# Optimization experiments

Hardware: AMD Instinct MI355X
Metric: run time of the kernel (lower is better)

The kernel has to match this reference:

```python
import jax, jax.numpy as jnp
import numpy as np

B, C, H, W = 4, 512, 32, 32
NUM_HEADS, DIM_HEAD = 16, 32
DIM_ATTN = NUM_HEADS * DIM_HEAD  # 512
N = H * W


def setup_inputs() -> dict:
    key = jax.random.key(0)
    ks = jax.random.split(key, 6)
    s = 0.02
    return {
        "x": jax.random.normal(ks[0], (B, C, H, W), jnp.float32),
        "w_qkv": jax.random.normal(ks[1], (3 * DIM_ATTN, C), jnp.float32) * s,
        "b_qkv": jax.random.normal(ks[2], (3 * DIM_ATTN,), jnp.float32) * s,
        "w_proj": jax.random.normal(ks[3], (C, DIM_ATTN), jnp.float32) * s,
        "b_proj": jax.random.normal(ks[4], (C,), jnp.float32) * s,
        "shared_rel_pos": jax.random.normal(ks[5], (1, NUM_HEADS, N, N), jnp.float32) * s,
    }


def reference(x, w_qkv, b_qkv, w_proj, b_proj, shared_rel_pos):
    b, c, h, w = x.shape
    n = h * w
    scale = DIM_HEAD ** -0.5
    # 1x1 conv == per-pixel matmul over channels
    qkv = jnp.einsum('bchw,oc->bohw', x, w_qkv) + b_qkv[None, :, None, None]
    # [B, heads, 3*dh, N] -> chunk along dim 2 (matches torch .chunk(3, dim=2))
    qkv = qkv.reshape(b, NUM_HEADS, 3 * DIM_HEAD, n)
    q, k, v = jnp.split(qkv, 3, axis=2)          # each [B, heads, dh, N]
    attn = jnp.einsum('bhdi,bhdj->bhij', q, k) * scale  # q^T @ k
    attn = attn + shared_rel_pos
    attn = jax.nn.softmax(attn, axis=-1)
    out = jnp.einsum('bhdj,bhij->bhdi', v, attn)  # v @ attn^T, [B, heads, dh, N]
    out = out.reshape(b, NUM_HEADS * DIM_HEAD, h, w)
    out = jnp.einsum('bchw,oc->bohw', out, w_proj) + b_proj[None, :, None, None]
    return out
```

## Files before the change

### kernel.cpp

```cpp
#include <hip/hip_runtime.h>
#include <cstdint>
#include <cstddef>

#define BATCH 4
#define CIN   512
#define NPIX  1024
#define HEADS 16
#define DH    32
#define DATTN 512
#define O_QKV 1536
#define PPAD  88

typedef unsigned short u16;
typedef __bf16 bf16x4 __attribute__((ext_vector_type(4)));
typedef __bf16 bf16x8 __attribute__((ext_vector_type(8)));
typedef float  f32x4  __attribute__((ext_vector_type(4)));

typedef const __attribute__((address_space(1))) void g1_t;
typedef __attribute__((address_space(3))) void l3_t;

#if defined(__has_builtin)
#if __has_builtin(__builtin_amdgcn_exp2f)
#define EXP2(x) __builtin_amdgcn_exp2f(x)
#endif
#endif
#ifndef EXP2
#define EXP2(x) __expf((x) * 0.6931471805599453f)
#endif

__device__ __forceinline__ u16 f2bf(float f) {
  unsigned u = __float_as_uint(f);
  u += 0x7fffu + ((u >> 16) & 1u);
  return (u16)(u >> 16);
}

__device__ __forceinline__ void gl_lds16(const void* gp, void* lp) {
  __builtin_amdgcn_global_load_lds((g1_t*)gp, (l3_t*)lp, 16, 0, 0);
}

__global__ __launch_bounds__(256) void prep_w(const float* __restrict__ w1,
                                              const float* __restrict__ w2,
                                              u16* __restrict__ o1,
                                              u16* __restrict__ o2) {
  const int idx = blockIdx.x * 256 + threadIdx.x;
  const int n1 = (O_QKV * CIN) >> 2;
  float4 v = (idx < n1) ? reinterpret_cast<const float4*>(w1)[idx]
                        : reinterpret_cast<const float4*>(w2)[idx - n1];
  uint2 pk = make_uint2((unsigned)f2bf(v.x) | ((unsigned)f2bf(v.y) << 16),
                        (unsigned)f2bf(v.z) | ((unsigned)f2bf(v.w) << 16));
  if (idx < n1) reinterpret_cast<uint2*>(o1)[idx] = pk;
  else          reinterpret_cast<uint2*>(o2)[idx - n1] = pk;
}

__global__ __launch_bounds__(256) void prep_x(const float* __restrict__ x,
                                              u16* __restrict__ xt) {
  __shared__ float sT[64][65];
  const int t  = threadIdx.x;
  const int n0 = blockIdx.x * 64;
  const int c0 = blockIdx.y * 64;
  const int b  = blockIdx.z;
  const float* xb = x + ((size_t)b * CIN + c0) * NPIX + n0;
#pragma unroll
  for (int i = 0; i < 4; ++i) {
    int r   = i * 16 + (t >> 4);
    int col = (t & 15) << 2;
    float4 v = *reinterpret_cast<const float4*>(&xb[(size_t)r * NPIX + col]);
    sT[r][col + 0] = v.x; sT[r][col + 1] = v.y;
    sT[r][col + 2] = v.z; sT[r][col + 3] = v.w;
  }
  __syncthreads();
#pragma unroll
  for (int i = 0; i < 2; ++i) {
    int nl = t >> 2;
    int ch = (t & 3) + (i << 2);
    u16 tmp[8];
#pragma unroll
    for (int e = 0; e < 8; ++e) tmp[e] = f2bf(sT[(ch << 3) + e][nl]);
    *reinterpret_cast<uint4*>(&xt[((size_t)b * NPIX + n0 + nl) * CIN + c0 + (ch << 3)]) =
        *reinterpret_cast<uint4*>(tmp);
  }
}

__global__ __launch_bounds__(256) void gemm_qkv_mfma(const u16* __restrict__ wq,
                                                     const u16* __restrict__ xt,
                                                     const float* __restrict__ bias,
                                                     u16* __restrict__ qt,
                                                     u16* __restrict__ kt,
                                                     u16* __restrict__ vt) {
  __shared__ __align__(16) u16 sA[96 * 64];
  __shared__ __align__(16) u16 sB[128 * 64];
  const int t  = threadIdx.x;
  const int w  = t >> 6, l = t & 63, g = l >> 4, ln = l & 15;
  const int n0 = blockIdx.x * 128;
  const int h  = blockIdx.y;
  const int b  = blockIdx.z;
  const int wm = w >> 1, wn = w & 1;

  const u16* wbase = wq + (size_t)h * 96 * CIN;
  const u16* xbase = xt + ((size_t)b * NPIX + n0) * CIN;

  f32x4 acc[3][4];
#pragma unroll
  for (int mi = 0; mi < 3; ++mi)
#pragma unroll
    for (int ni = 0; ni < 4; ++ni) acc[mi][ni] = {0.f, 0.f, 0.f, 0.f};

  for (int k0 = 0; k0 < CIN; k0 += 64) {
#pragma unroll
    for (int i = 0; i < 3; ++i) {
      int chunk = i * 256 + (w << 6) + l;
      gl_lds16(wbase + ((size_t)(chunk >> 3)) * CIN + k0 + ((chunk & 7) << 3),
               (char*)sA + i * 4096 + (w << 10));
    }
#pragma unroll
    for (int i = 0; i < 4; ++i) {
      int chunk = i * 256 + (w << 6) + l;
      gl_lds16(xbase + ((size_t)(chunk >> 3)) * CIN + k0 + ((chunk & 7) << 3),
               (char*)sB + i * 4096 + (w << 10));
    }
    __syncthreads();
#pragma unroll
    for (int kk = 0; kk < 64; kk += 32) {
      bf16x8 af[3], bfr[4];
#pragma unroll
      for (int mi = 0; mi < 3; ++mi)
        af[mi] = *reinterpret_cast<const bf16x8*>(&sA[(48 * wm + 16 * mi + ln) * 64 + kk + (g << 3)]);
#pragma unroll
      for (int ni = 0; ni < 4; ++ni)
        bfr[ni] = *reinterpret_cast<const bf16x8*>(&sB[((wn << 6) + (ni << 4) + ln) * 64 + kk + (g << 3)]);
#pragma unroll
      for (int mi = 0; mi < 3; ++mi)
#pragma unroll
        for (int ni = 0; ni < 4; ++ni)
          acc[mi][ni] = __builtin_amdgcn_mfma_f32_16x16x32_bf16(af[mi], bfr[ni], acc[mi][ni], 0, 0, 0);
    }
    __syncthreads();
  }

  const float QSC = 0.17677669529663687f * 1.4426950408889634f;
  const float* bh = bias + h * 96;
#pragma unroll
  for (int mi = 0; mi < 3; ++mi) {
    const int sec = 48 * wm + 16 * mi;
    const int rb  = sec + (g << 2);
    const float b0 = bh[rb + 0], b1 = bh[rb + 1], b2 = bh[rb + 2], b3 = bh[rb + 3];
#pragma unroll
    for (int ni = 0; ni < 4; ++ni) {
      const int n = n0 + (wn << 6) + (ni << 4) + ln;
      f32x4 a = acc[mi][ni];
      float v0 = a[0] + b0, v1 = a[1] + b1, v2 = a[2] + b2, v3 = a[3] + b3;
      if (sec < 32) { v0 *= QSC; v1 *= QSC; v2 *= QSC; v3 *= QSC; }
      u16 e0 = f2bf(v0), e1 = f2bf(v1), e2 = f2bf(v2), e3 = f2bf(v3);
      if (sec < 32) {
        const int d = sec + (g << 2);
        uint2 pk = make_uint2((unsigned)e0 | ((unsigned)e1 << 16),
                              (unsigned)e2 | ((unsigned)e3 << 16));
        *reinterpret_cast<uint2*>(&qt[(((size_t)(b * HEADS + h)) * NPIX + n) * DH + d]) = pk;
      } else if (sec < 64) {
        const int d = sec - 32 + (g << 2);
        uint2 pk = make_uint2((unsigned)e0 | ((unsigned)e1 << 16),
                              (unsigned)e2 | ((unsigned)e3 << 16));
        *reinterpret_cast<uint2*>(&kt[(((size_t)(b * HEADS + h)) * NPIX + n) * DH + d]) = pk;
      } else {
        const int d = sec - 64 + (g << 2);
        u16* vp = &vt[(((size_t)(b * HEADS + h)) * DH + d) * NPIX + n];
        vp[0] = e0; vp[NPIX] = e1; vp[2 * NPIX] = e2; vp[3 * NPIX] = e3;
      }
    }
  }
}

__global__ __launch_bounds__(512, 4) void attn_mfma(const u16* __restrict__ qt,
                                                    const u16* __restrict__ kt,
                                                    const u16* __restrict__ vt,
                                                    const float* __restrict__ rel,
                                                    u16* __restrict__ aout) {
  __shared__ __align__(16) u16 sK[2][2 * 2048];
  __shared__ __align__(16) u16 sV[2][2 * 2048];
  __shared__ __align__(16) u16 sP[8][16 * PPAD];

  const int t  = threadIdx.x;
  const int w  = t >> 6, l = t & 63, g = l >> 4, ln = l & 15;
  const int bid = blockIdx.x;
  const int xcd = bid & 7, sl = bid >> 3;
  const int h   = (xcd << 1) | (sl >> 5);
  const int i0  = ((sl >> 1) & 15) << 6;
  const int bp  = sl & 1;
  const int bw  = (bp << 1) | (w >> 2);
  const int iw  = w & 3;
  const float LOG2E = 1.4426950408889634f;

  bf16x8 qf = *reinterpret_cast<const bf16x8*>(
      qt + (((size_t)(bw * HEADS + h)) * NPIX + i0 + (iw << 4) + ln) * DH + (g << 3));

  f32x4 vzero = {0.f, 0.f, 0.f, 0.f};
  f32x4 accO[2] = {vzero, vzero};
  float l_lane[4] = {0.f, 0.f, 0.f, 0.f};

  const int sc_b  = (bp << 1) | (t >> 8);
  const int sc_cb = t & 255;
  const int sc_r  = sc_cb >> 3;
  const int sc_kc = (sc_cb & 7) ^ (sc_r & 7) ^ ((sc_r >> 3) & 1);
  const int sc_vc = (sc_cb & 7) ^ (sc_r & 7);
  const u16* ksrc0 = kt + (((size_t)(sc_b * HEADS + h)) * NPIX +
                           ((sc_r << 1) | (sc_kc >> 2))) * DH + ((sc_kc & 3) << 3);
  const u16* vsrc0 = vt + (((size_t)(sc_b * HEADS + h)) * DH + sc_r) * NPIX + (sc_vc << 3);

#define STAGE(js_, p_) do {                                               \
    gl_lds16(ksrc0 + (size_t)(js_) * 2048, (char*)&sK[p_][0] + (w << 10)); \
    gl_lds16(vsrc0 + (size_t)(js_) * 64,   (char*)&sV[p_][0] + (w << 10)); \
  } while (0)

  const float* relp = rel + ((size_t)h * NPIX + i0 + (iw << 4) + (g << 2)) * NPIX + (ln << 2);
  f32x4 relA4[4], relB4[4];
#pragma unroll
  for (int v = 0; v < 4; ++v)
    relA4[v] = *reinterpret_cast<const f32x4*>(relp + (size_t)v * NPIX);

  STAGE(0, 0);

  u16* sPw = &sP[w][0];
  const int lb = w >> 2;

  for (int js = 0; js < 16; ++js) {
    const int p = js & 1;
    __syncthreads();
    if (js < 15) {
      STAGE(js + 1, p ^ 1);
#pragma unroll
      for (int v = 0; v < 4; ++v)
        relB4[v] = *reinterpret_cast<const f32x4*>(relp + (size_t)v * NPIX + ((js + 1) << 6));
    }

    const u16* Kb = &sK[p][lb << 11];
    const u16* Vb = &sV[p][lb << 11];

    f32x4 sfr[4];
#pragma unroll
    for (int jj = 0; jj < 4; ++jj) {
      const int r  = (ln << 1) + (jj >> 1);
      const int ks = ((((jj & 1) << 2) | g) ^ (r & 7)) ^ ((r >> 3) & 1);
      bf16x8 kf = *reinterpret_cast<const bf16x8*>(Kb + r * 64 + ks * 8);
      sfr[jj] = __builtin_amdgcn_mfma_f32_16x16x32_bf16(qf, kf, vzero, 0, 0, 0);
    }

#pragma unroll
    for (int v = 0; v < 4; ++v) {
      float p0 = EXP2(fmaf(relA4[v][0], LOG2E, sfr[0][v]));
      float p1 = EXP2(fmaf(relA4[v][1], LOG2E, sfr[1][v]));
      float p2 = EXP2(fmaf(relA4[v][2], LOG2E, sfr[2][v]));
      float p3 = EXP2(fmaf(relA4[v][3], LOG2E, sfr[3][v]));
      l_lane[v] += (p0 + p1) + (p2 + p3);
      bf16x4 pk;
      pk[0] = (__bf16)p0; pk[1] = (__bf16)p1; pk[2] = (__bf16)p2; pk[3] = (__bf16)p3;
      *reinterpret_cast<bf16x4*>(sPw + ((g << 2) + v) * PPAD + (ln << 2)) = pk;
    }

#pragma unroll
    for (int kc = 0; kc < 2; ++kc) {
      bf16x8 pa = *reinterpret_cast<const bf16x8*>(sPw + ln * PPAD + (kc << 5) + (g << 3));
#pragma unroll
      for (int dc = 0; dc < 2; ++dc) {
        const int d  = (dc << 4) + ln;
        const int vs = ((kc << 2) | g) ^ (d & 7);
        bf16x8 vf = *reinterpret_cast<const bf16x8*>(Vb + d * 64 + vs * 8);
        accO[dc] = __builtin_amdgcn_mfma_f32_16x16x32_bf16(pa, vf, accO[dc], 0, 0, 0);
      }
    }

    if (js < 15) {
#pragma unroll
      for (int v = 0; v < 4; ++v) relA4[v] = relB4[v];
    }
  }
#undef STAGE

#pragma unroll
  for (int v = 0; v < 4; ++v) {
    float ls = l_lane[v];
    ls += __shfl_xor(ls, 1);
    ls += __shfl_xor(ls, 2);
    ls += __shfl_xor(ls, 4);
    ls += __shfl_xor(ls, 8);
    const float inv = 1.f / ls;
    const size_t row = (size_t)bw * NPIX + i0 + (iw << 4) + (g << 2) + v;
    aout[row * DATTN + (h << 5) + ln]      = f2bf(accO[0][v] * inv);
    aout[row * DATTN + (h << 5) + 16 + ln] = f2bf(accO[1][v] * inv);
  }
}

__global__ __launch_bounds__(256) void gemm_proj_mfma(const u16* __restrict__ wp,
                                                      const u16* __restrict__ at,
                                                      const float* __restrict__ bias,
                                                      float* __restrict__ out) {
  __shared__ __align__(16) u16 sA[64 * 64];
  __shared__ __align__(16) u16 sB[128 * 64];
  const int t  = threadIdx.x;
  const int w  = t >> 6, l = t & 63, g = l >> 4, ln = l & 15;
  const int n0 = blockIdx.x * 128;
  const int o0 = blockIdx.y * 64;
  const int b  = blockIdx.z;
  const int wm = w >> 1, wn = w & 1;

  const u16* wbase = wp + (size_t)o0 * DATTN;
  const u16* abase = at + ((size_t)b * NPIX + n0) * DATTN;

  f32x4 acc[2][4];
#pragma unroll
  for (int mi = 0; mi < 2; ++mi)
#pragma unroll
    for (int ni = 0; ni < 4; ++ni) acc[mi][ni] = {0.f, 0.f, 0.f, 0.f};

  for (int k0 = 0; k0 < DATTN; k0 += 64) {
#pragma unroll
    for (int i = 0; i < 2; ++i) {
      int chunk = i * 256 + (w << 6) + l;
      gl_lds16(wbase + ((size_t)(chunk >> 3)) * DATTN + k0 + ((chunk & 7) << 3),
               (char*)sA + i * 4096 + (w << 10));
    }
#pragma unroll
    for (int i = 0; i < 4; ++i) {
      int chunk = i * 256 + (w << 6) + l;
      gl_lds16(abase + ((size_t)(chunk >> 3)) * DATTN + k0 + ((chunk & 7) << 3),
               (char*)sB + i * 4096 + (w << 10));
    }
    __syncthreads();
#pragma unroll
    for (int kk = 0; kk < 64; kk += 32) {
      bf16x8 af[2], bfr[4];
#pragma unroll
      for (int mi = 0; mi < 2; ++mi)
        af[mi] = *reinterpret_cast<const bf16x8*>(&sA[((wm << 5) + (mi << 4) + ln) * 64 + kk + (g << 3)]);
#pragma unroll
      for (int ni = 0; ni < 4; ++ni)
        bfr[ni] = *reinterpret_cast<const bf16x8*>(&sB[((wn << 6) + (ni << 4) + ln) * 64 + kk + (g << 3)]);
#pragma unroll
      for (int mi = 0; mi < 2; ++mi)
#pragma unroll
        for (int ni = 0; ni < 4; ++ni)
          acc[mi][ni] = __builtin_amdgcn_mfma_f32_16x16x32_bf16(af[mi], bfr[ni], acc[mi][ni], 0, 0, 0);
    }
    __syncthreads();
  }

#pragma unroll
  for (int mi = 0; mi < 2; ++mi) {
    const int o = o0 + (wm << 5) + (mi << 4) + (g << 2);
    const float b0 = bias[o], b1 = bias[o + 1], b2 = bias[o + 2], b3 = bias[o + 3];
#pragma unroll
    for (int ni = 0; ni < 4; ++ni) {
      const int n = n0 + (wn << 6) + (ni << 4) + ln;
      float* op = &out[((size_t)b * DATTN + o) * NPIX + n];
      op[0]        = acc[mi][ni][0] + b0;
      op[NPIX]     = acc[mi][ni][1] + b1;
      op[2 * NPIX] = acc[mi][ni][2] + b2;
      op[3 * NPIX] = acc[mi][ni][3] + b3;
    }
  }
}

extern "C" void kernel_launch(void* const* d_in, const int* in_sizes, int n_in,
                              void* d_out, int out_size, void* d_ws, size_t ws_size,
                              hipStream_t stream) {
  (void)in_sizes; (void)n_in; (void)out_size; (void)ws_size;
  const float* x      = (const float*)d_in[0];
  const float* w_qkv  = (const float*)d_in[1];
  const float* b_qkv  = (const float*)d_in[2];
  const float* w_proj = (const float*)d_in[3];
  const float* b_proj = (const float*)d_in[4];
  const float* rel    = (const float*)d_in[5];
  float* out = (float*)d_out;

  u16* xt    = (u16*)d_ws;
  u16* wq_bf = xt + (size_t)BATCH * NPIX * CIN;
  u16* wp_bf = wq_bf + (size_t)O_QKV * CIN;
  u16* qt    = wp_bf + (size_t)DATTN * DATTN;
  u16* kt    = qt + (size_t)BATCH * HEADS * NPIX * DH;
  u16* vt    = kt + (size_t)BATCH * HEADS * NPIX * DH;
  u16* aout  = vt + (size_t)BATCH * HEADS * NPIX * DH;

  prep_w<<<1024, 256, 0, stream>>>(w_qkv, w_proj, wq_bf, wp_bf);
  prep_x<<<dim3(NPIX / 64, CIN / 64, BATCH), 256, 0, stream>>>(x, xt);
  gemm_qkv_mfma<<<dim3(NPIX / 128, HEADS, BATCH), 256, 0, stream>>>(wq_bf, xt, b_qkv, qt, kt, vt);
  attn_mfma<<<512, 512, 0, stream>>>(qt, kt, vt, rel, aout);
  gemm_proj_mfma<<<dim3(NPIX / 128, DATTN / 64, BATCH), 256, 0, stream>>>(wp_bf, aout, b_proj, out);
}
```

Measured before the change: 66.18 us.

## Split attention key range across wave halves and merge partial results in LDS

```diff
diff --git a/kernel.cpp b/kernel.cpp
--- a/kernel.cpp
+++ b/kernel.cpp
@@ -9,7 +9,6 @@
 #define DH    32
 #define DATTN 512
 #define O_QKV 1536
-#define PPAD  88
 
 typedef unsigned short u16;
 typedef __bf16 bf16x4 __attribute__((ext_vector_type(4)));
@@ -170,70 +169,81 @@
   }
 }
 
-__global__ __launch_bounds__(512, 4) void attn_mfma(const u16* __restrict__ qt,
+__global__ __launch_bounds__(512, 6) void attn_mfma(const u16* __restrict__ qt,
                                                     const u16* __restrict__ kt,
                                                     const u16* __restrict__ vt,
                                                     const float* __restrict__ rel,
                                                     u16* __restrict__ aout) {
-  __shared__ __align__(16) u16 sK[2][2 * 2048];
-  __shared__ __align__(16) u16 sV[2][2 * 2048];
-  __shared__ __align__(16) u16 sP[8][16 * PPAD];
+  __shared__ __align__(16) u16 sK[2][2][2048];
+  __shared__ __align__(16) u16 sV[2][2][2048];
+  __shared__ __align__(16) u16 sP[8][1024];
 
   const int t  = threadIdx.x;
   const int w  = t >> 6, l = t & 63, g = l >> 4, ln = l & 15;
   const int bid = blockIdx.x;
-  const int xcd = bid & 7, sl = bid >> 3;
-  const int h   = (xcd << 1) | (sl >> 5);
-  const int i0  = ((sl >> 1) & 15) << 6;
-  const int bp  = sl & 1;
-  const int bw  = (bp << 1) | (w >> 2);
+  const int xcd = bid & 7;
+  const int idx = bid >> 3;
+  const int b   = idx & 3;
+  const int grp = idx >> 2;
+  const int h   = (xcd << 1) | (grp >> 4);
+  const int i0  = (grp & 15) << 6;
   const int iw  = w & 3;
-  const float LOG2E = 1.4426950408889634f;
+  const int jh  = w >> 2;
+
+  const size_t bh = (size_t)(b * HEADS + h);
+
+  const int lr = l >> 3, ls = l & 7;
+  const int kcl = ls ^ lr ^ (iw & 1);
+  const int kj  = (iw << 4) + (lr << 1) + (kcl >> 2);
+  const u16* ksrc = kt + (bh * NPIX + (jh << 9) + kj) * DH + ((kcl & 3) << 3);
+  const int vcl = ls ^ lr;
+  const int vd  = (iw << 3) + lr;
+  const u16* vsrc = vt + (bh * DH + vd) * NPIX + (jh << 9) + (vcl << 3);
+  char* kdst = (char*)&sK[0][jh][0] + (iw << 10);
+  char* vdst = (char*)&sV[0][jh][0] + (iw << 10);
+
+#define STAGE(s_, p_) do {                                          \
+    gl_lds16(ksrc + (size_t)(s_) * 2048, kdst + (p_) * 8192);       \
+    gl_lds16(vsrc + (size_t)(s_) * 64,   vdst + (p_) * 8192);       \
+  } while (0)
+
+  STAGE(0, 0);
+  __builtin_amdgcn_sched_barrier(0);
 
   bf16x8 qf = *reinterpret_cast<const bf16x8*>(
-      qt + (((size_t)(bw * HEADS + h)) * NPIX + i0 + (iw << 4) + ln) * DH + (g << 3));
+      qt + (bh * NPIX + i0 + (iw << 4) + ln) * DH + (g << 3));
+
+  const float* relp = rel + ((size_t)h * NPIX + i0 + (iw << 4) + (g << 2)) * NPIX +
+                      (jh << 9) + (ln << 2);
+  f32x4 relbuf[2][4];
+#pragma unroll
+  for (int v = 0; v < 4; ++v)
+    relbuf[0][v] = *reinterpret_cast<const f32x4*>(relp + (size_t)v * NPIX);
+  __builtin_amdgcn_sched_barrier(0);
 
   f32x4 vzero = {0.f, 0.f, 0.f, 0.f};
   f32x4 accO[2] = {vzero, vzero};
-  float l_lane[4] = {0.f, 0.f, 0.f, 0.f};
-
-  const int sc_b  = (bp << 1) | (t >> 8);
-  const int sc_cb = t & 255;
-  const int sc_r  = sc_cb >> 3;
-  const int sc_kc = (sc_cb & 7) ^ (sc_r & 7) ^ ((sc_r >> 3) & 1);
-  const int sc_vc = (sc_cb & 7) ^ (sc_r & 7);
-  const u16* ksrc0 = kt + (((size_t)(sc_b * HEADS + h)) * NPIX +
-                           ((sc_r << 1) | (sc_kc >> 2))) * DH + ((sc_kc & 3) << 3);
-  const u16* vsrc0 = vt + (((size_t)(sc_b * HEADS + h)) * DH + sc_r) * NPIX + (sc_vc << 3);
-
-#define STAGE(js_, p_) do {                                               \
-    gl_lds16(ksrc0 + (size_t)(js_) * 2048, (char*)&sK[p_][0] + (w << 10)); \
-    gl_lds16(vsrc0 + (size_t)(js_) * 64,   (char*)&sV[p_][0] + (w << 10)); \
-  } while (0)
-
-  const float* relp = rel + ((size_t)h * NPIX + i0 + (iw << 4) + (g << 2)) * NPIX + (ln << 2);
-  f32x4 relA4[4], relB4[4];
-#pragma unroll
-  for (int v = 0; v < 4; ++v)
-    relA4[v] = *reinterpret_cast<const f32x4*>(relp + (size_t)v * NPIX);
-
-  STAGE(0, 0);
+  f32x4 l_lane = vzero;
 
   u16* sPw = &sP[w][0];
-  const int lb = w >> 2;
-
-  for (int js = 0; js < 16; ++js) {
-    const int p = js & 1;
-    __syncthreads();
-    if (js < 15) {
-      STAGE(js + 1, p ^ 1);
+
+#pragma unroll
+  for (int s = 0; s < 8; ++s) {
+    const int p = s & 1;
+    asm volatile("s_waitcnt vmcnt(4)" ::: "memory");
+    __builtin_amdgcn_s_barrier();
+    __builtin_amdgcn_sched_barrier(0);
+    if (s < 7) {
+      STAGE(s + 1, p ^ 1);
 #pragma unroll
       for (int v = 0; v < 4; ++v)
-        relB4[v] = *reinterpret_cast<const f32x4*>(relp + (size_t)v * NPIX + ((js + 1) << 6));
-    }
-
-    const u16* Kb = &sK[p][lb << 11];
-    const u16* Vb = &sV[p][lb << 11];
+        relbuf[(s + 1) & 1][v] =
+            *reinterpret_cast<const f32x4*>(relp + (size_t)v * NPIX + ((s + 1) << 6));
+    }
+    __builtin_amdgcn_sched_barrier(0);
+
+    const u16* Kb = &sK[p][jh][0];
+    const u16* Vb = &sV[p][jh][0];
 
     f32x4 sfr[4];
 #pragma unroll
@@ -244,48 +254,62 @@
       sfr[jj] = __builtin_amdgcn_mfma_f32_16x16x32_bf16(qf, kf, vzero, 0, 0, 0);
     }
 
+    const float LOG2E = 1.4426950408889634f;
 #pragma unroll
     for (int v = 0; v < 4; ++v) {
-      float p0 = EXP2(fmaf(relA4[v][0], LOG2E, sfr[0][v]));
-      float p1 = EXP2(fmaf(relA4[v][1], LOG2E, sfr[1][v]));
-      float p2 = EXP2(fmaf(relA4[v][2], LOG2E, sfr[2][v]));
-      float p3 = EXP2(fmaf(relA4[v][3], LOG2E, sfr[3][v]));
+      float p0 = EXP2(fmaf(relbuf[p][v][0], LOG2E, sfr[0][v]));
+      float p1 = EXP2(fmaf(relbuf[p][v][1], LOG2E, sfr[1][v]));
+      float p2 = EXP2(fmaf(relbuf[p][v][2], LOG2E, sfr[2][v]));
+      float p3 = EXP2(fmaf(relbuf[p][v][3], LOG2E, sfr[3][v]));
       l_lane[v] += (p0 + p1) + (p2 + p3);
       bf16x4 pk;
       pk[0] = (__bf16)p0; pk[1] = (__bf16)p1; pk[2] = (__bf16)p2; pk[3] = (__bf16)p3;
-      *reinterpret_cast<bf16x4*>(sPw + ((g << 2) + v) * PPAD + (ln << 2)) = pk;
+      const int rw = (g << 2) + v;
+      *reinterpret_cast<bf16x4*>(
+          sPw + rw * 64 + ((((ln >> 1) ^ (rw & 7)) << 3) | ((ln & 1) << 2))) = pk;
     }
 
 #pragma unroll
     for (int kc = 0; kc < 2; ++kc) {
-      bf16x8 pa = *reinterpret_cast<const bf16x8*>(sPw + ln * PPAD + (kc << 5) + (g << 3));
+      const int lc = (kc << 2) | g;
+      bf16x8 pa = *reinterpret_cast<const bf16x8*>(sPw + ln * 64 + ((lc ^ (ln & 7)) << 3));
 #pragma unroll
       for (int dc = 0; dc < 2; ++dc) {
         const int d  = (dc << 4) + ln;
-        const int vs = ((kc << 2) | g) ^ (d & 7);
+        const int vs = lc ^ (d & 7);
         bf16x8 vf = *reinterpret_cast<const bf16x8*>(Vb + d * 64 + vs * 8);
         accO[dc] = __builtin_amdgcn_mfma_f32_16x16x32_bf16(pa, vf, accO[dc], 0, 0, 0);
       }
     }
-
-    if (js < 15) {
-#pragma unroll
-      for (int v = 0; v < 4; ++v) relA4[v] = relB4[v];
-    }
   }
 #undef STAGE
 
-#pragma unroll
-  for (int v = 0; v < 4; ++v) {
-    float ls = l_lane[v];
-    ls += __shfl_xor(ls, 1);
-    ls += __shfl_xor(ls, 2);
-    ls += __shfl_xor(ls, 4);
-    ls += __shfl_xor(ls, 8);
-    const float inv = 1.f / ls;
-    const size_t row = (size_t)bw * NPIX + i0 + (iw << 4) + (g << 2) + v;
-    aout[row * DATTN + (h << 5) + ln]      = f2bf(accO[0][v] * inv);
-    aout[row * DATTN + (h << 5) + 16 + ln] = f2bf(accO[1][v] * inv);
+  __syncthreads();
+  float* mrg = (float*)&sK[0][0][0];
+  if (jh == 1) {
+    float* mp = mrg + ((size_t)((iw << 6) + l)) * 12;
+    *reinterpret_cast<f32x4*>(mp + 0) = accO[0];
+    *reinterpret_cast<f32x4*>(mp + 4) = accO[1];
+    *reinterpret_cast<f32x4*>(mp + 8) = l_lane;
+  }
+  __syncthreads();
+  if (jh == 0) {
+    const float* mp = mrg + ((size_t)((iw << 6) + l)) * 12;
+    f32x4 o0 = accO[0] + *reinterpret_cast<const f32x4*>(mp + 0);
+    f32x4 o1 = accO[1] + *reinterpret_cast<const f32x4*>(mp + 4);
+    f32x4 lv = l_lane + *reinterpret_cast<const f32x4*>(mp + 8);
+#pragma unroll
+    for (int v = 0; v < 4; ++v) {
+      float ls = lv[v];
+      ls += __shfl_xor(ls, 1);
+      ls += __shfl_xor(ls, 2);
+      ls += __shfl_xor(ls, 4);
+      ls += __shfl_xor(ls, 8);
+      const float inv = 1.f / ls;
+      const size_t row = (size_t)b * NPIX + i0 + (iw << 4) + (g << 2) + v;
+      aout[row * DATTN + (h << 5) + ln]      = f2bf(o0[v] * inv);
+      aout[row * DATTN + (h << 5) + 16 + ln] = f2bf(o1[v] * inv);
+    }
   }
 }
 
@@ -382,6 +406,6 @@
   prep_w<<<1024, 256, 0, stream>>>(w_qkv, w_proj, wq_bf, wp_bf);
   prep_x<<<dim3(NPIX / 64, CIN / 64, BATCH), 256, 0, stream>>>(x, xt);
   gemm_qkv_mfma<<<dim3(NPIX / 128, HEADS, BATCH), 256, 0, stream>>>(wq_bf, xt, b_qkv, qt, kt, vt);
-  attn_mfma<<<512, 512, 0, stream>>>(qt, kt, vt, rel, aout);
+  attn_mfma<<<1024, 512, 0, stream>>>(qt, kt, vt, rel, aout);
   gemm_proj_mfma<<<dim3(NPIX / 128, DATTN / 64, BATCH), 256, 0, stream>>>(wp_bf, aout, b_proj, out);
 }
```

Result: slower. 124.0 us (+87.3%).

## Drop LDS staging of K/V in attention, load fragments directly from global

Applied to the files above, without the earlier changes.

```diff
diff --git a/kernel.cpp b/kernel.cpp
--- a/kernel.cpp
+++ b/kernel.cpp
@@ -9,7 +9,6 @@
 #define DH    32
 #define DATTN 512
 #define O_QKV 1536
-#define PPAD  88
 
 typedef unsigned short u16;
 typedef __bf16 bf16x4 __attribute__((ext_vector_type(4)));
@@ -170,110 +169,188 @@
   }
 }
 
-__global__ __launch_bounds__(512, 4) void attn_mfma(const u16* __restrict__ qt,
+__global__ __launch_bounds__(256, 4) void attn_mfma(const u16* __restrict__ qt,
                                                     const u16* __restrict__ kt,
                                                     const u16* __restrict__ vt,
                                                     const float* __restrict__ rel,
                                                     u16* __restrict__ aout) {
-  __shared__ __align__(16) u16 sK[2][2 * 2048];
-  __shared__ __align__(16) u16 sV[2][2 * 2048];
-  __shared__ __align__(16) u16 sP[8][16 * PPAD];
+  __shared__ __align__(16) u16 sP[4][1024];
 
   const int t  = threadIdx.x;
   const int w  = t >> 6, l = t & 63, g = l >> 4, ln = l & 15;
   const int bid = blockIdx.x;
   const int xcd = bid & 7, sl = bid >> 3;
-  const int h   = (xcd << 1) | (sl >> 5);
-  const int i0  = ((sl >> 1) & 15) << 6;
-  const int bp  = sl & 1;
-  const int bw  = (bp << 1) | (w >> 2);
-  const int iw  = w & 3;
-  const float LOG2E = 1.4426950408889634f;
+  const int b   = sl & 3;
+  const int i0  = ((sl >> 2) & 15) << 6;
+  const int h   = (xcd << 1) | (sl >> 6);
+  const int iw  = w;
+
+  const size_t bh = (size_t)(b * HEADS + h);
+
+  const u16* kbase = kt + (bh * NPIX + (ln << 2)) * DH + (g << 3);
+  const u16* vbase0 = vt + (bh * DH + ln) * NPIX + (g << 3);
+  const u16* vbase1 = vbase0 + 16 * NPIX;
+  const float* relp = rel + ((size_t)h * NPIX + i0 + (iw << 4) + (g << 2)) * NPIX +
+                      (ln << 2);
 
   bf16x8 qf = *reinterpret_cast<const bf16x8*>(
-      qt + (((size_t)(bw * HEADS + h)) * NPIX + i0 + (iw << 4) + ln) * DH + (g << 3));
+      qt + (bh * NPIX + i0 + (iw << 4) + ln) * DH + (g << 3));
 
   f32x4 vzero = {0.f, 0.f, 0.f, 0.f};
   f32x4 accO[2] = {vzero, vzero};
-  float l_lane[4] = {0.f, 0.f, 0.f, 0.f};
-
-  const int sc_b  = (bp << 1) | (t >> 8);
-  const int sc_cb = t & 255;
-  const int sc_r  = sc_cb >> 3;
-  const int sc_kc = (sc_cb & 7) ^ (sc_r & 7) ^ ((sc_r >> 3) & 1);
-  const int sc_vc = (sc_cb & 7) ^ (sc_r & 7);
-  const u16* ksrc0 = kt + (((size_t)(sc_b * HEADS + h)) * NPIX +
-                           ((sc_r << 1) | (sc_kc >> 2))) * DH + ((sc_kc & 3) << 3);
-  const u16* vsrc0 = vt + (((size_t)(sc_b * HEADS + h)) * DH + sc_r) * NPIX + (sc_vc << 3);
-
-#define STAGE(js_, p_) do {                                               \
-    gl_lds16(ksrc0 + (size_t)(js_) * 2048, (char*)&sK[p_][0] + (w << 10)); \
-    gl_lds16(vsrc0 + (size_t)(js_) * 64,   (char*)&sV[p_][0] + (w << 10)); \
+  f32x4 l_lane = vzero;
+
+  u16* sPw = &sP[w][0];
+  const float LOG2E = 1.4426950408889634f;
+
+  f32x4 ra0 = *reinterpret_cast<const f32x4*>(relp);
+  f32x4 ra1 = *reinterpret_cast<const f32x4*>(relp + NPIX);
+  f32x4 ra2 = *reinterpret_cast<const f32x4*>(relp + 2 * NPIX);
+  f32x4 ra3 = *reinterpret_cast<const f32x4*>(relp + 3 * NPIX);
+  f32x4 rb0 = vzero, rb1 = vzero, rb2 = vzero, rb3 = vzero;
+
+#define STEP(s_, R0, R1, R2, R3, RN0, RN1, RN2, RN3)                          \
+  do {                                                                         \
+    const int s = (s_);                                                        \
+                     \
+    const u16* kp = kbase + (size_t)s * 2048;                                  \
+    bf16x8 kf0 = *reinterpret_cast<const bf16x8*>(kp);                         \
+    bf16x8 kf1 = *reinterpret_cast<const bf16x8*>(kp + 32);                    \
+    bf16x8 kf2 = *reinterpret_cast<const bf16x8*>(kp + 64);                    \
+    bf16x8 kf3 = *reinterpret_cast<const bf16x8*>(kp + 96);                    \
+                               \
+    const u16* vp0 = vbase0 + (size_t)s * 64;                                  \
+    const u16* vp1 = vbase1 + (size_t)s * 64;                                  \
+    bf16x8 vf00 = *reinterpret_cast<const bf16x8*>(vp0);                       \
+    bf16x8 vf10 = *reinterpret_cast<const bf16x8*>(vp0 + 32);                  \
+    bf16x8 vf01 = *reinterpret_cast<const bf16x8*>(vp1);                       \
+    bf16x8 vf11 = *reinterpret_cast<const bf16x8*>(vp1 + 32);                  \
+                            \
+    if (s < 15) {                                                              \
+      const float* rn = relp + (size_t)(s + 1) * 64;                           \
+      RN0 = *reinterpret_cast<const f32x4*>(rn);                               \
+      RN1 = *reinterpret_cast<const f32x4*>(rn + NPIX);                        \
+      RN2 = *reinterpret_cast<const f32x4*>(rn + 2 * NPIX);                    \
+      RN3 = *reinterpret_cast<const f32x4*>(rn + 3 * NPIX);                    \
+    }                                                                          \
+                       \
+    f32x4 sfr0, sfr1, sfr2, sfr3;                                              \
+    __builtin_amdgcn_s_setprio(1);                                             \
+    sfr0 = __builtin_amdgcn_mfma_f32_16x16x32_bf16(qf, kf0, vzero, 0, 0, 0);   \
+    sfr1 = __builtin_amdgcn_mfma_f32_16x16x32_bf16(qf, kf1, vzero, 0, 0, 0);   \
+    sfr2 = __builtin_amdgcn_mfma_f32_16x16x32_bf16(qf, kf2, vzero, 0, 0, 0);   \
+    sfr3 = __builtin_amdgcn_mfma_f32_16x16x32_bf16(qf, kf3, vzero, 0, 0, 0);   \
+    __builtin_amdgcn_s_setprio(0);                                             \
+                     \
+    _Pragma("unroll")                                                          \
+    for (int v = 0; v < 4; ++v) {                                              \
+      float p0 = EXP2(fmaf(R0[v], LOG2E, sfr0[v]));                            \
+      float p1 = EXP2(fmaf(R1[v], LOG2E, sfr1[v]));                            \
+      float p2 = EXP2(fmaf(R2[v], LOG2E, sfr2[v]));                            \
+      float p3 = EXP2(fmaf(R3[v], LOG2E, sfr3[v]));                            \
+                             \
+      l_lane[v] += (p0 + p1) + (p2 + p3);                                      \
+      bf16x4 pk;                                                               \
+      pk[0] = (__bf16)p0; pk[1] = (__bf16)p1;                                  \
+      pk[2] = (__bf16)p2; pk[3] = (__bf16)p3;                                  \
+      const int rw = (g << 2) + v;                                             \
+      *reinterpret_cast<bf16x4*>(                                              \
+          sPw + rw * 64 + ((((ln >> 1) ^ (rw & 7)) << 3) | ((ln & 1) << 2))) = pk; \
+    }                                                                          \
+                                         \
+    __builtin_amdgcn_s_setprio(1);                                             \
+    {                                                                          \
+      bf16x8 pa0 = *reinterpret_cast<const bf16x8*>(sPw + ln * 64 + ((g ^ (ln & 7)) << 3)); \
+      accO[0] = __builtin_amdgcn_mfma_f32_16x16x32_bf16(pa0, vf00, accO[0], 0, 0, 0); \
+      accO[1] = __builtin_amdgcn_mfma_f32_16x16x32_bf16(pa0, vf01, accO[1], 0, 0, 0); \
+      bf16x8 pa1 = *reinterpret_cast<const bf16x8*>(sPw + ln * 64 + (((4 | g) ^ (ln & 7)) << 3)); \
+      accO[0] = __builtin_amdgcn_mfma_f32_16x16x32_bf16(pa1, vf10, accO[0], 0, 0, 0); \
+      accO[1] = __builtin_amdgcn_mfma_f32_16x16x32_bf16(pa1, vf11, accO[1], 0, 0, 0); \
+    }                                                                          \
+    __builtin_amdgcn_s_setprio(0);                                             \
   } while (0)
 
-  const float* relp = rel + ((size_t)h * NPIX + i0 + (iw << 4) + (g << 2)) * NPIX + (ln << 2);
-  f32x4 relA4[4], relB4[4];
-#pragma unroll
-  for (int v = 0; v < 4; ++v)
-    relA4[v] = *reinterpret_cast<const f32x4*>(relp + (size_t)v * NPIX);
-
-  STAGE(0, 0);
-
-  u16* sPw = &sP[w][0];
-  const int lb = w >> 2;
-
-  for (int js = 0; js < 16; ++js) {
-    const int p = js & 1;
-    __syncthreads();
-    if (js < 15) {
-      STAGE(js + 1, p ^ 1);
-#pragma unroll
-      for (int v = 0; v < 4; ++v)
-        relB4[v] = *reinterpret_cast<const f32x4*>(relp + (size_t)v * NPIX + ((js + 1) << 6));
-    }
-
-    const u16* Kb = &sK[p][lb << 11];
-    const u16* Vb = &sV[p][lb << 11];
-
-    f32x4 sfr[4];
-#pragma unroll
-    for (int jj = 0; jj < 4; ++jj) {
-      const int r  = (ln << 1) + (jj >> 1);
-      const int ks = ((((jj & 1) << 2) | g) ^ (r & 7)) ^ ((r >> 3) & 1);
-      bf16x8 kf = *reinterpret_cast<const bf16x8*>(Kb + r * 64 + ks * 8);
-      sfr[jj] = __builtin_amdgcn_mfma_f32_16x16x32_bf16(qf, kf, vzero, 0, 0, 0);
-    }
-
-#pragma unroll
-    for (int v = 0; v < 4; ++v) {
-      float p0 = EXP2(fmaf(relA4[v][0], LOG2E, sfr[0][v]));
-      float p1 = EXP2(fmaf(relA4[v][1], LOG2E, sfr[1][v]));
-      float p2 = EXP2(fmaf(relA4[v][2], LOG2E, sfr[2][v]));
-      float p3 = EXP2(fmaf(relA4[v][3], LOG2E, sfr[3][v]));
-      l_lane[v] += (p0 + p1) + (p2 + p3);
-      bf16x4 pk;
-      pk[0] = (__bf16)p0; pk[1] = (__bf16)p1; pk[2] = (__bf16)p2; pk[3] = (__bf16)p3;
-      *reinterpret_cast<bf16x4*>(sPw + ((g << 2) + v) * PPAD + (ln << 2)) = pk;
-    }
-
-#pragma unroll
-    for (int kc = 0; kc < 2; ++kc) {
-      bf16x8 pa = *reinterpret_cast<const bf16x8*>(sPw + ln * PPAD + (kc << 5) + (g << 3));
-#pragma unroll
-      for (int dc = 0; dc < 2; ++dc) {
-        const int d  = (dc << 4) + ln;
-        const int vs = ((kc << 2) | g) ^ (d & 7);
-        bf16x8 vf = *reinterpret_cast<const bf16x8*>(Vb + d * 64 + vs * 8);
-        accO[dc] = __builtin_amdgcn_mfma_f32_16x16x32_bf16(pa, vf, accO[dc], 0, 0, 0);
-      }
-    }
-
-    if (js < 15) {
-#pragma unroll
-      for (int v = 0; v < 4; ++v) relA4[v] = relB4[v];
-    }
-  }
-#undef STAGE
+#undef STEP
+#define STEP(s_, R0, R1, R2, R3, RN0, RN1, RN2, RN3)                          \
+  do {                                                                         \
+    const int s = (s_);                                                        \
+    const u16* kp = kbase + (size_t)s * 2048;                                  \
+    bf16x8 kf0 = *reinterpret_cast<const bf16x8*>(kp);                         \
+    bf16x8 kf1 = *reinterpret_cast<const bf16x8*>(kp + 32);                    \
+    bf16x8 kf2 = *reinterpret_cast<const bf16x8*>(kp + 64);                    \
+    bf16x8 kf3 = *reinterpret_cast<const bf16x8*>(kp + 96);                    \
+    const u16* vp0 = vbase0 + (size_t)s * 64;                                  \
+    const u16* vp1 = vbase1 + (size_t)s * 64;                                  \
+    bf16x8 vf00 = *reinterpret_cast<const bf16x8*>(vp0);                       \
+    bf16x8 vf10 = *reinterpret_cast<const bf16x8*>(vp0 + 32);                  \
+    bf16x8 vf01 = *reinterpret_cast<const bf16x8*>(vp1);                       \
+    bf16x8 vf11 = *reinterpret_cast<const bf16x8*>(vp1 + 32);                  \
+    if (s < 15) {                                                              \
+      const float* rn = relp + (size_t)(s + 1) * 64;                           \
+      RN0 = *reinterpret_cast<const f32x4*>(rn);                               \
+      RN1 = *reinterpret_cast<const f32x4*>(rn + NPIX);                        \
+      RN2 = *reinterpret_cast<const f32x4*>(rn + 2 * NPIX);                    \
+      RN3 = *reinterpret_cast<const f32x4*>(rn + 3 * NPIX);                    \
+    }                                                                          \
+    f32x4 sfr0, sfr1, sfr2, sfr3;                                              \
+    __builtin_amdgcn_s_setprio(1);                                             \
+    sfr0 = __builtin_amdgcn_mfma_f32_16x16x32_bf16(qf, kf0, vzero, 0, 0, 0);   \
+    sfr1 = __builtin_amdgcn_mfma_f32_16x16x32_bf16(qf, kf1, vzero, 0, 0, 0);   \
+    sfr2 = __builtin_amdgcn_mfma_f32_16x16x32_bf16(qf, kf2, vzero, 0, 0, 0);   \
+    sfr3 = __builtin_amdgcn_mfma_f32_16x16x32_bf16(qf, kf3, vzero, 0, 0, 0);   \
+    __builtin_amdgcn_s_setprio(0);                                             \
+    {                                                                          \
+      float p0, p1, p2, p3; bf16x4 pk; int rw;                                 \
+      p0 = EXP2(fmaf(R0[0], LOG2E, sfr0[0]));                                  \
+      p1 = EXP2(fmaf(R0[1], LOG2E, sfr1[0]));                                  \
+      p2 = EXP2(fmaf(R0[2], LOG2E, sfr2[0]));                                  \
+      p3 = EXP2(fmaf(R0[3], LOG2E, sfr3[0]));                                  \
+      l_lane[0] += (p0 + p1) + (p2 + p3);                                      \
+      pk[0] = (__bf16)p0; pk[1] = (__bf16)p1; pk[2] = (__bf16)p2; pk[3] = (__bf16)p3; \
+      rw = (g << 2) + 0;                                                       \
+      *reinterpret_cast<bf16x4*>(sPw + rw * 64 + ((((ln >> 1) ^ (rw & 7)) << 3) | ((ln & 1) << 2))) = pk; \
+      p0 = EXP2(fmaf(R1[0], LOG2E, sfr0[1]));                                  \
+      p1 = EXP2(fmaf(R1[1], LOG2E, sfr1[1]));                                  \
+      p2 = EXP2(fmaf(R1[2], LOG2E, sfr2[1]));                                  \
+      p3 = EXP2(fmaf(R1[3], LOG2E, sfr3[1]));                                  \
+      l_lane[1] += (p0 + p1) + (p2 + p3);                                      \
+      pk[0] = (__bf16)p0; pk[1] = (__bf16)p1; pk[2] = (__bf16)p2; pk[3] = (__bf16)p3; \
+      rw = (g << 2) + 1;                                                       \
+      *reinterpret_cast<bf16x4*>(sPw + rw * 64 + ((((ln >> 1) ^ (rw & 7)) << 3) | ((ln & 1) << 2))) = pk; \
+      p0 = EXP2(fmaf(R2[0], LOG2E, sfr0[2]));                                  \
+      p1 = EXP2(fmaf(R2[1], LOG2E, sfr1[2]));                                  \
+      p2 = EXP2(fmaf(R2[2], LOG2E, sfr2[2]));                                  \
+      p3 = EXP2(fmaf(R2[3], LOG2E, sfr3[2]));                                  \
+      l_lane[2] += (p0 + p1) + (p2 + p3);                                      \
+      pk[0] = (__bf16)p0; pk[1] = (__bf16)p1; pk[2] = (__bf16)p2; pk[3] = (__bf16)p3; \
+      rw = (g << 2) + 2;                                                       \
+      *reinterpret_cast<bf16x4*>(sPw + rw * 64 + ((((ln >> 1) ^ (rw & 7)) << 3) | ((ln & 1) << 2))) = pk; \
+      p0 = EXP2(fmaf(R3[0], LOG2E, sfr0[3]));                                  \
+      p1 = EXP2(fmaf(R3[1], LOG2E, sfr1[3]));                                  \
+      p2 = EXP2(fmaf(R3[2], LOG2E, sfr2[3]));                                  \
+      p3 = EXP2(fmaf(R3[3], LOG2E, sfr3[3]));                                  \
+      l_lane[3] += (p0 + p1) + (p2 + p3);                                      \
+      pk[0] = (__bf16)p0; pk[1] = (__bf16)p1; pk[2] = (__bf16)p2; pk[3] = (__bf16)p3; \
+      rw = (g << 2) + 3;                                                       \
+      *reinterpret_cast<bf16x4*>(sPw + rw * 64 + ((((ln >> 1) ^ (rw & 7)) << 3) | ((ln & 1) << 2))) = pk; \
+    }                                                                          \
+    __builtin_amdgcn_s_setprio(1);                                             \
+    {                                                                          \
+      bf16x8 pa0 = *reinterpret_cast<const bf16x8*>(sPw + ln * 64 + ((g ^ (ln & 7)) << 3)); \
+      accO[0] = __builtin_amdgcn_mfma_f32_16x16x32_bf16(pa0, vf00, accO[0], 0, 0, 0); \
+      accO[1] = __builtin_amdgcn_mfma_f32_16x16x32_bf16(pa0, vf01, accO[1], 0, 0, 0); \
+      bf16x8 pa1 = *reinterpret_cast<const bf16x8*>(sPw + ln * 64 + (((4 | g) ^ (ln & 7)) << 3)); \
+      accO[0] = __builtin_amdgcn_mfma_f32_16x16x32_bf16(pa1, vf10, accO[0], 0, 0, 0); \
+      accO[1] = __builtin_amdgcn_mfma_f32_16x16x32_bf16(pa1, vf11, accO[1], 0, 0, 0); \
+    }                                                                          \
+    __builtin_amdgcn_s_setprio(0);                                             \
+  } while (0)
+
+  for (int s2 = 0; s2 < 8; ++s2) {
+    STEP(2 * s2,     ra0, ra1, ra2, ra3, rb0, rb1, rb2, rb3);
+    STEP(2 * s2 + 1, rb0, rb1, rb2, rb3, ra0, ra1, ra2, ra3);
+  }
+#undef STEP
 
 #pragma unroll
   for (int v = 0; v < 4; ++v) {
@@ -283,7 +360,7 @@
     ls += __shfl_xor(ls, 4);
     ls += __shfl_xor(ls, 8);
     const float inv = 1.f / ls;
-    const size_t row = (size_t)bw * NPIX + i0 + (iw << 4) + (g << 2) + v;
+    const size_t row = (size_t)b * NPIX + i0 + (iw << 4) + (g << 2) + v;
     aout[row * DATTN + (h << 5) + ln]      = f2bf(accO[0][v] * inv);
     aout[row * DATTN + (h << 5) + 16 + ln] = f2bf(accO[1][v] * inv);
   }
@@ -382,6 +459,6 @@
   prep_w<<<1024, 256, 0, stream>>>(w_qkv, w_proj, wq_bf, wp_bf);
   prep_x<<<dim3(NPIX / 64, CIN / 64, BATCH), 256, 0, stream>>>(x, xt);
   gemm_qkv_mfma<<<dim3(NPIX / 128, HEADS, BATCH), 256, 0, stream>>>(wq_bf, xt, b_qkv, qt, kt, vt);
-  attn_mfma<<<512, 512, 0, stream>>>(qt, kt, vt, rel, aout);
+  attn_mfma<<<1024, 256, 0, stream>>>(qt, kt, vt, rel, aout);
   gemm_proj_mfma<<<dim3(NPIX / 128, DATTN / 64, BATCH), 256, 0, stream>>>(wp_bf, aout, b_proj, out);
 }
```

Measured after the change: 121.9 us. 84.2% more time.
